# Kernel tuning notes

Hardware: AMD Instinct MI355X
Metric: run time of the kernel (lower is better)

The kernel has to match this reference:

```python
import jax, jax.numpy as jnp
import numpy as np

P = 113          # modulus; eq_token = P, vocab = P + 1
D_MODEL = 1024
D_MLP = 4096
BATCH = 16384


def setup_inputs() -> dict:
    key = jax.random.key(0)
    ks = jax.random.split(key, 9)
    return {
        "a": jax.random.randint(ks[0], (BATCH,), 0, P, dtype=jnp.int64 if jax.config.jax_enable_x64 else jnp.int32),
        "b": jax.random.randint(ks[1], (BATCH,), 0, P, dtype=jnp.int64 if jax.config.jax_enable_x64 else jnp.int32),
        "token_embed": jax.random.normal(ks[2], (P + 1, D_MODEL), dtype=jnp.float32),
        "pos_embed": jax.random.normal(ks[3], (3, D_MODEL), dtype=jnp.float32),
        "W_in_w": jax.random.normal(ks[4], (D_MLP, D_MODEL), dtype=jnp.float32) * (1.0 / np.sqrt(D_MODEL)),
        "W_in_b": jax.random.normal(ks[5], (D_MLP,), dtype=jnp.float32) * 0.02,
        "W_out_w": jax.random.normal(ks[6], (D_MODEL, D_MLP), dtype=jnp.float32) * (1.0 / np.sqrt(D_MLP)),
        "W_out_b": jax.random.normal(ks[7], (D_MODEL,), dtype=jnp.float32) * 0.02,
        "unembed_w": jax.random.normal(ks[8], (P, D_MODEL), dtype=jnp.float32) * (1.0 / np.sqrt(D_MODEL)),
    }


def reference(a, b, token_embed, pos_embed, W_in_w, W_in_b, W_out_w, W_out_b, unembed_w):
    # tokens: (batch, 3) = [a, b, eq]
    eq = jnp.full_like(a, P)
    tokens = jnp.stack([a, b, eq], axis=1)
    # embed + positional: (batch, 3, d_model)
    x = token_embed[tokens] + pos_embed[None, :, :]
    # FNet-style mixing: FFT over seq (axis 1), then over d_model (axis 2), real part
    wave = jnp.fft.fft(jnp.fft.fft(x, axis=1), axis=2).real.astype(x.dtype)
    x = x + wave
    # MLP with residual
    h = jax.nn.relu(jnp.einsum('bsd,md->bsm', x, W_in_w) + W_in_b)
    x = x + jnp.einsum('bsm,dm->bsd', h, W_out_w) + W_out_b
    # unembed only the '=' position (index 2)
    logits = jnp.einsum('bd,vd->bv', x[:, 2, :], unembed_w)
    return logits
```

## Files before the change

### kernel.cpp

```cpp
#include <hip/hip_runtime.h>

typedef __attribute__((ext_vector_type(4))) float f32x4;
typedef __attribute__((ext_vector_type(8))) short short8;

#define PMOD 113
#define NPAIR 12769
#define DM 1024
#define DMLP 4096
#define NBATCH 16384
#define SQRT3_2 0.86602540378443865f
#define CSTEP 6.1359231515425649e-3f
#define LTSTRIDE (12800 * 128)
#define NZ 8

__device__ __forceinline__ short f2bf(float x) {
    unsigned int u = __builtin_bit_cast(unsigned int, x);
    u += 0x7FFFu + ((u >> 16) & 1u);
    return (short)(u >> 16);
}
__device__ __forceinline__ float bf2f(short s) {
    return __builtin_bit_cast(float, (unsigned int)(unsigned short)s << 16);
}
__device__ __forceinline__ void cvt16(const float* p, short8& o0, short8& o1) {
    #pragma unroll
    for (int c4 = 0; c4 < 4; ++c4) {
        f32x4 v = *(const f32x4*)(p + c4 * 4);
        #pragma unroll
        for (int e = 0; e < 4; ++e) {
            short s = f2bf(v[e]);
            if (c4 < 2) o0[c4 * 4 + e] = s; else o1[(c4 - 2) * 4 + e] = s;
        }
    }
}

__global__ __launch_bounds__(256) void k_prep(
    unsigned short* __restrict__ Fb, unsigned short* __restrict__ V2b,
    unsigned short* __restrict__ Wob,
    const float* __restrict__ E, const float* __restrict__ pos,
    const float* __restrict__ Wo)
{
    __shared__ float smem[64 * 65];
    const int blk = blockIdx.x, tid = threadIdx.x;

    if (blk < 1024) {
        const int f = blk;
        for (int k = tid; k < DM; k += 256) {
            float v;
            if (k <= 512) v = cosf((float)((f * k) & 1023) * CSTEP);
            else          v = sinf((float)((f * (k - 512)) & 1023) * CSTEP);
            Fb[f * DM + k] = (unsigned short)f2bf(v);
        }
    } else if (blk < 1252) {
        const int t = blk - 1024;
        if (t >= 226) {
            for (int k = tid; k < DM; k += 256) V2b[t * DM + k] = 0;
            return;
        }
        float* vc = smem;
        float* vs = smem + 1024;
        if (t < PMOD) {
            const float* e = E + t * DM;
            const float* e2 = E + PMOD * DM;
            for (int d = tid; d < DM; d += 256) {
                float e2v = e2[d] + pos[2 * DM + d];
                vc[d] = e[d] + pos[d] - 0.5f * pos[DM + d] - 0.5f * e2v;
                vs[d] = SQRT3_2 * (pos[DM + d] - e2v);
            }
        } else {
            const float* e = E + (t - PMOD) * DM;
            for (int d = tid; d < DM; d += 256) {
                float x = e[d];
                vc[d] = -0.5f * x;
                vs[d] = SQRT3_2 * x;
            }
        }
        __syncthreads();
        for (int k = tid; k < DM; k += 256) {
            float o;
            if (k == 0)        o = vc[0];
            else if (k < 512)  o = vc[k] + vc[1024 - k];
            else if (k == 512) o = vc[512];
            else               o = vs[k - 512] - vs[1536 - k];
            V2b[t * DM + k] = (unsigned short)f2bf(o);
        }
    } else {
        const int idx = blk - 1252;
        const int m0 = (idx & 63) * 64;
        const int d0 = (idx >> 6) * 64;
        float (*tile)[65] = (float(*)[65])smem;
        #pragma unroll
        for (int it = 0; it < 16; ++it) {
            int i2 = tid + it * 256;
            int r = i2 >> 6, c = i2 & 63;
            tile[c][r] = Wo[(d0 + r) * DMLP + m0 + c];
        }
        __syncthreads();
        #pragma unroll
        for (int it = 0; it < 16; ++it) {
            int i2 = tid + it * 256;
            int r = i2 >> 6, c = i2 & 63;
            Wob[(m0 + r) * DM + d0 + c] = (unsigned short)f2bf(tile[r][c]);
        }
    }
}

template<int MODE>
__device__ __forceinline__ void mfma_body(
    int n0, int row0,
    unsigned short* __restrict__ C1, float* __restrict__ C2,
    const void* __restrict__ Av, const void* __restrict__ B1v,
    const float* __restrict__ B2, const float* __restrict__ bias,
    const float* __restrict__ E, const float* __restrict__ pos,
    const float* __restrict__ bo, short* sA, short* sB)
{
    const int tid = threadIdx.x;
    const int sr = tid >> 2, sq = (tid & 3) * 16;
    const int lane = tid & 63, w = tid >> 6;
    const int wr = w >> 1, wc = w & 1;
    const int lr = lane & 15, lg = lane >> 4;

    const unsigned short* Ab = nullptr; const float* Af = nullptr;
    {
        int r = row0 + sr;
        if (MODE == 2) { if (r < PMOD) Af = (const float*)Av + r * DM; }
        else           { if (r < 228)  Ab = (const unsigned short*)Av + r * DM; }
    }
    const unsigned short* Bb = nullptr; const float* Bf = nullptr;
    {
        int n = n0 + sr;
        if (MODE == 1) {
            if (n < 4096) Bf = (const float*)B1v + n * DM;
            else if (n - 4096 < PMOD) Bf = B2 + (n - 4096) * DM;
        } else {
            Bb = (const unsigned short*)B1v + n * DM;
        }
    }

    f32x4 acc[2][2];
    #pragma unroll
    for (int i = 0; i < 2; ++i)
        #pragma unroll
        for (int j = 0; j < 2; ++j) acc[i][j] = 0.f;

    for (int k0 = 0; k0 < DM; k0 += 64) {
        short8 a0, a1, b0, b1;
        if (MODE == 2) {
            if (Af) cvt16(Af + k0 + sq, a0, a1);
            else { a0 = 0; a1 = 0; }
        } else {
            if (Ab) { a0 = ((const short8*)(Ab + k0 + sq))[0];
                      a1 = ((const short8*)(Ab + k0 + sq))[1]; }
            else { a0 = 0; a1 = 0; }
        }
        if (MODE == 1) {
            if (Bf) cvt16(Bf + k0 + sq, b0, b1);
            else { b0 = 0; b1 = 0; }
        } else {
            b0 = ((const short8*)(Bb + k0 + sq))[0];
            b1 = ((const short8*)(Bb + k0 + sq))[1];
        }
        if (k0) __syncthreads();
        *(short8*)&sA[sr * 72 + sq] = a0;
        *(short8*)&sA[sr * 72 + sq + 8] = a1;
        *(short8*)&sB[sr * 72 + sq] = b0;
        *(short8*)&sB[sr * 72 + sq + 8] = b1;
        __syncthreads();

        #pragma unroll
        for (int ks = 0; ks < 2; ++ks) {
            short8 af[2], bfr[2];
            #pragma unroll
            for (int i = 0; i < 2; ++i)
                af[i] = *(const short8*)&sA[(wr * 32 + i * 16 + lr) * 72 + ks * 32 + lg * 8];
            #pragma unroll
            for (int j = 0; j < 2; ++j)
                bfr[j] = *(const short8*)&sB[(wc * 32 + j * 16 + lr) * 72 + ks * 32 + lg * 8];
            #pragma unroll
            for (int i = 0; i < 2; ++i)
                #pragma unroll
                for (int j = 0; j < 2; ++j)
                    acc[i][j] = __builtin_amdgcn_mfma_f32_16x16x32_bf16(af[i], bfr[j], acc[i][j], 0, 0, 0);
        }
    }

    #pragma unroll
    for (int i = 0; i < 2; ++i) {
        #pragma unroll
        for (int q = 0; q < 4; ++q) {
            int r = row0 + wr * 32 + i * 16 + lg * 4 + q;
            #pragma unroll
            for (int j = 0; j < 2; ++j) {
                int cg = n0 + wc * 32 + j * 16 + lr;
                float v = acc[i][j][q];
                if (MODE == 0) {
                    if (r < 228) {
                        if (r < PMOD) v += E[PMOD * DM + cg] + pos[2 * DM + cg];
                        if (r == 227) v += bo[cg];
                        C1[r * DM + cg] = (unsigned short)f2bf(v);
                    }
                } else if (MODE == 1) {
                    if (r < 228) {
                        if (n0 < 4096) {
                            if (r < PMOD) v += bias[cg];
                            C1[r * DMLP + cg] = (unsigned short)f2bf(v);
                        } else {
                            C2[r * 128 + cg - 4096] = v;
                        }
                    }
                } else {
                    if (r < 128) C1[r * DMLP + cg] = (unsigned short)f2bf(v);
                }
            }
        }
    }
}

__global__ __launch_bounds__(256) void k_m02(
    unsigned short* __restrict__ Tb, unsigned short* __restrict__ Mb,
    const unsigned short* __restrict__ V2b, const unsigned short* __restrict__ Fb,
    const float* __restrict__ U, const unsigned short* __restrict__ Wob,
    const float* __restrict__ E, const float* __restrict__ pos,
    const float* __restrict__ bo)
{
    __shared__ short sA[64 * 72];
    __shared__ short sB[64 * 72];
    const int blk = blockIdx.x;
    if (blk < 64) {
        mfma_body<0>((blk & 15) * 64, (blk >> 4) * 64, Tb, nullptr, V2b, Fb,
                     nullptr, nullptr, E, pos, bo, sA, sB);
    } else {
        int i = blk - 64;
        mfma_body<2>((i & 63) * 64, (i >> 6) * 64, Mb, nullptr, U, Wob,
                     nullptr, nullptr, nullptr, nullptr, nullptr, sA, sB);
    }
}

__global__ __launch_bounds__(256) void k_m1(
    unsigned short* __restrict__ Hb, float* __restrict__ L,
    const unsigned short* __restrict__ Tb, const float* __restrict__ Wi,
    const float* __restrict__ U, const float* __restrict__ bi)
{
    __shared__ short sA[64 * 72];
    __shared__ short sB[64 * 72];
    mfma_body<1>(blockIdx.x * 64, blockIdx.y * 64, Hb, L, Tb, Wi, U, bi,
                 nullptr, nullptr, nullptr, sA, sB);
}

__global__ __launch_bounds__(256) void k_pair_gemm(
    unsigned short* __restrict__ LTp,
    const unsigned short* __restrict__ Hb,
    const unsigned short* __restrict__ Mb,
    const float* __restrict__ L)
{
    __shared__ short sH[128 * 72];
    __shared__ short sM[128 * 72];

    const int tid = threadIdx.x;
    const int p0 = blockIdx.x * 128;
    const int z = blockIdx.y;
    const int kbeg = z * 512;
    const bool slice0 = (z == 0);
    unsigned short* outp = LTp + (size_t)z * LTSTRIDE;

    const int hr = tid >> 1, kh = (tid & 1) * 32;
    {
    }
    const unsigned int pc = (unsigned)min(p0 + hr, NPAIR - 1);
    const unsigned int a_r = pc / 113u;
    const unsigned int b_r = pc - a_r * 113u;
    const unsigned short* pHA = Hb + a_r * DMLP + kbeg + kh;
    const unsigned short* pHB = Hb + (PMOD + b_r) * DMLP + kbeg + kh;
    const unsigned short* pM  = Mb + hr * DMLP + kbeg + kh;

    const int lane = tid & 63, w = tid >> 6;
    const int wr = w >> 1, wc = w & 1;
    const int lr = lane & 15, lg = lane >> 4;

    f32x4 acc[4][4];
    #pragma unroll
    for (int i = 0; i < 4; ++i)
        #pragma unroll
        for (int j = 0; j < 4; ++j) acc[i][j] = 0.f;

    short8 rA[4], rB[4], rM[4];
    #pragma unroll
    for (int c = 0; c < 4; ++c) {
        rA[c] = *(const short8*)(pHA + c * 8);
        rB[c] = *(const short8*)(pHB + c * 8);
        rM[c] = *(const short8*)(pM + c * 8);
    }

    #pragma unroll 1
    for (int t = 0; t < 8; ++t) {
        short8 u[4];
        #pragma unroll
        for (int c = 0; c < 4; ++c)
            #pragma unroll
            for (int e = 0; e < 8; ++e)
                u[c][e] = f2bf(fmaxf(bf2f(rA[c][e]) + bf2f(rB[c][e]), 0.f));

        if (t) __syncthreads();
        #pragma unroll
        for (int c = 0; c < 4; ++c) {
            *(short8*)&sH[hr * 72 + kh + c * 8] = u[c];
            *(short8*)&sM[hr * 72 + kh + c * 8] = rM[c];
        }
        __syncthreads();

        if (t < 7) {
            #pragma unroll
            for (int c = 0; c < 4; ++c) {
                rA[c] = *(const short8*)(pHA + (t + 1) * 64 + c * 8);
                rB[c] = *(const short8*)(pHB + (t + 1) * 64 + c * 8);
                rM[c] = *(const short8*)(pM + (t + 1) * 64 + c * 8);
            }
        }

        #pragma unroll
        for (int ks = 0; ks < 2; ++ks) {
            short8 af[4], bf[4];
            #pragma unroll
            for (int i = 0; i < 4; ++i)
                af[i] = *(const short8*)&sH[(wr * 64 + i * 16 + lr) * 72 + ks * 32 + lg * 8];
            #pragma unroll
            for (int j = 0; j < 4; ++j)
                bf[j] = *(const short8*)&sM[(wc * 64 + j * 16 + lr) * 72 + ks * 32 + lg * 8];
            #pragma unroll
            for (int i = 0; i < 4; ++i)
                #pragma unroll
                for (int j = 0; j < 4; ++j)
                    acc[i][j] = __builtin_amdgcn_mfma_f32_16x16x32_bf16(af[i], bf[j], acc[i][j], 0, 0, 0);
        }
    }

    const float* Lb0 = L + PMOD * 128;
    const float* Lc = L + 227 * 128;
    #pragma unroll
    for (int i = 0; i < 4; ++i) {
        #pragma unroll
        for (int q = 0; q < 4; ++q) {
            int p = p0 + wr * 64 + i * 16 + lg * 4 + q;
            if (p >= NPAIR) continue;
            unsigned int pa = (unsigned)p / 113u;
            unsigned int pb = (unsigned)p - pa * 113u;
            unsigned short* dst = outp + (size_t)p * 128;
            const float* La = L + pa * 128;
            const float* Lb = Lb0 + pb * 128;
            #pragma unroll
            for (int j = 0; j < 4; ++j) {
                int col = wc * 64 + j * 16 + lr;
                float val = acc[i][j][q];
                if (slice0) val += La[col] + Lb[col] + Lc[col];
                dst[col] = (unsigned short)f2bf(val);
            }
        }
    }
}

__global__ __launch_bounds__(256) void k_gather(
    float* __restrict__ out, const unsigned short* __restrict__ LTp,
    const int* __restrict__ a, const int* __restrict__ b)
{
    int g = blockIdx.x * 256 + threadIdx.x;
    if (g >= NBATCH * PMOD) return;
    unsigned int i = (unsigned)g / 113u;
    unsigned int v = (unsigned)g - i * 113u;
    size_t off = (size_t)((unsigned)a[i] * 113u + (unsigned)b[i]) * 128 + v;
    float s = 0.f;
    #pragma unroll
    for (int z = 0; z < NZ; ++z)
        s += bf2f(LTp[(size_t)z * LTSTRIDE + off]);
    out[g] = s;
}

extern "C" void kernel_launch(void* const* d_in, const int* in_sizes, int n_in,
                              void* d_out, int out_size, void* d_ws, size_t ws_size,
                              hipStream_t stream)
{
    const int*   a   = (const int*)d_in[0];
    const int*   b   = (const int*)d_in[1];
    const float* E   = (const float*)d_in[2];
    const float* pos = (const float*)d_in[3];
    const float* Wi  = (const float*)d_in[4];
    const float* bi  = (const float*)d_in[5];
    const float* Wo  = (const float*)d_in[6];
    const float* bo  = (const float*)d_in[7];
    const float* U   = (const float*)d_in[8];
    float* out = (float*)d_out;

    unsigned short* Fb  = (unsigned short*)d_ws;
    unsigned short* V2b = Fb + 1024 * 1024;
    unsigned short* Tb  = V2b + 228 * 1024;
    unsigned short* Hb  = Tb + 228 * 1024;
    unsigned short* Wob = Hb + 228 * 4096;
    unsigned short* Mb  = Wob + 4096 * 1024;
    unsigned short* LTp = Mb + 128 * 4096;
    float* L = (float*)(LTp + NZ * LTSTRIDE);

    k_prep<<<2276, 256, 0, stream>>>(Fb, V2b, Wob, E, pos, Wo);
    k_m02<<<192, 256, 0, stream>>>(Tb, Mb, V2b, Fb, U, Wob, E, pos, bo);
    k_m1<<<dim3(66, 4), 256, 0, stream>>>(Hb, L, Tb, Wi, U, bi);
    k_pair_gemm<<<dim3(100, NZ), 256, 0, stream>>>(LTp, Hb, Mb, L);
    k_gather<<<(NBATCH * PMOD + 255) / 256, 256, 0, stream>>>(out, LTp, a, b);

    (void)in_sizes; (void)n_in; (void)out_size; (void)ws_size;
}
```

Baseline: 176.7 us.

## Pre-convert Wi/U to bf16, split-K the first MLP GEMM, and interleave partial-logit layout

Moves fp32-to-bf16 conversion of W_in and unembed into the prep kernel so the GEMM inner loops load bf16 directly. Splits the k_m1 GEMM into four K-slices for more blocks (264 to 1056) and adds a reduction kernel that sums the partials, adds the bias and writes Hb and L. Reorders the pair-GEMM output so the NZ partial slices of each pair are contiguous, and rewrites the gather to read them with 16-byte vector loads. This trades an extra kernel launch and fp32 partial-buffer traffic for better occupancy and more coalesced gathers.

```diff
diff --git a/kernel.cpp b/kernel.cpp
--- a/kernel.cpp
+++ b/kernel.cpp
@@ -2,6 +2,7 @@
 
 typedef __attribute__((ext_vector_type(4))) float f32x4;
 typedef __attribute__((ext_vector_type(8))) short short8;
+typedef __attribute__((ext_vector_type(4))) unsigned short us4;
 
 #define PMOD 113
 #define NPAIR 12769
@@ -10,8 +11,8 @@
 #define NBATCH 16384
 #define SQRT3_2 0.86602540378443865f
 #define CSTEP 6.1359231515425649e-3f
-#define LTSTRIDE (12800 * 128)
 #define NZ 8
+#define HPELEMS (228 * 4224)
 
 __device__ __forceinline__ short f2bf(float x) {
     unsigned int u = __builtin_bit_cast(unsigned int, x);
@@ -35,9 +36,11 @@
 
 __global__ __launch_bounds__(256) void k_prep(
     unsigned short* __restrict__ Fb, unsigned short* __restrict__ V2b,
-    unsigned short* __restrict__ Wob,
+    unsigned short* __restrict__ Wob, unsigned short* __restrict__ Wib,
+    unsigned short* __restrict__ Ub,
     const float* __restrict__ E, const float* __restrict__ pos,
-    const float* __restrict__ Wo)
+    const float* __restrict__ Wo, const float* __restrict__ Wi,
+    const float* __restrict__ U)
 {
     __shared__ float smem[64 * 65];
     const int blk = blockIdx.x, tid = threadIdx.x;
@@ -83,7 +86,7 @@
             else               o = vs[k - 512] - vs[1536 - k];
             V2b[t * DM + k] = (unsigned short)f2bf(o);
         }
-    } else {
+    } else if (blk < 2276) {
         const int idx = blk - 1252;
         const int m0 = (idx & 63) * 64;
         const int d0 = (idx >> 6) * 64;
@@ -101,15 +104,29 @@
             int r = i2 >> 6, c = i2 & 63;
             Wob[(m0 + r) * DM + d0 + c] = (unsigned short)f2bf(tile[r][c]);
         }
+    } else if (blk < 3300) {
+        const int eb = (blk - 2276) * 4096 + tid * 16;
+        short8 o0, o1;
+        cvt16(Wi + eb, o0, o1);
+        *(short8*)&Wib[eb] = o0;
+        *(short8*)&Wib[eb + 8] = o1;
+    } else {
+        const int eb = (blk - 3300) * 4096 + tid * 16;
+        if (eb < PMOD * DM) {
+            short8 o0, o1;
+            cvt16(U + eb, o0, o1);
+            *(short8*)&Ub[eb] = o0;
+            *(short8*)&Ub[eb + 8] = o1;
+        }
     }
 }
 
 template<int MODE>
 __device__ __forceinline__ void mfma_body(
-    int n0, int row0,
-    unsigned short* __restrict__ C1, float* __restrict__ C2,
-    const void* __restrict__ Av, const void* __restrict__ B1v,
-    const float* __restrict__ B2, const float* __restrict__ bias,
+    int n0, int row0, int kbeg, int kend, int Arows,
+    unsigned short* __restrict__ C1, float* __restrict__ C2f,
+    const unsigned short* __restrict__ A, const unsigned short* __restrict__ B1,
+    const unsigned short* __restrict__ B2,
     const float* __restrict__ E, const float* __restrict__ pos,
     const float* __restrict__ bo, short* sA, short* sB)
 {
@@ -119,20 +136,16 @@
     const int wr = w >> 1, wc = w & 1;
     const int lr = lane & 15, lg = lane >> 4;
 
-    const unsigned short* Ab = nullptr; const float* Af = nullptr;
-    {
-        int r = row0 + sr;
-        if (MODE == 2) { if (r < PMOD) Af = (const float*)Av + r * DM; }
-        else           { if (r < 228)  Ab = (const unsigned short*)Av + r * DM; }
-    }
-    const unsigned short* Bb = nullptr; const float* Bf = nullptr;
+    const unsigned short* Ab = (row0 + sr < Arows) ? (A + (row0 + sr) * DM) : nullptr;
+    const unsigned short* Bb;
     {
         int n = n0 + sr;
         if (MODE == 1) {
-            if (n < 4096) Bf = (const float*)B1v + n * DM;
-            else if (n - 4096 < PMOD) Bf = B2 + (n - 4096) * DM;
+            if (n < 4096) Bb = B1 + n * DM;
+            else if (n - 4096 < PMOD) Bb = B2 + (n - 4096) * DM;
+            else Bb = nullptr;
         } else {
-            Bb = (const unsigned short*)B1v + n * DM;
+            Bb = B1 + n * DM;
         }
     }
 
@@ -142,24 +155,15 @@
         #pragma unroll
         for (int j = 0; j < 2; ++j) acc[i][j] = 0.f;
 
-    for (int k0 = 0; k0 < DM; k0 += 64) {
+    for (int k0 = kbeg; k0 < kend; k0 += 64) {
         short8 a0, a1, b0, b1;
-        if (MODE == 2) {
-            if (Af) cvt16(Af + k0 + sq, a0, a1);
-            else { a0 = 0; a1 = 0; }
-        } else {
-            if (Ab) { a0 = ((const short8*)(Ab + k0 + sq))[0];
-                      a1 = ((const short8*)(Ab + k0 + sq))[1]; }
-            else { a0 = 0; a1 = 0; }
-        }
-        if (MODE == 1) {
-            if (Bf) cvt16(Bf + k0 + sq, b0, b1);
-            else { b0 = 0; b1 = 0; }
-        } else {
-            b0 = ((const short8*)(Bb + k0 + sq))[0];
-            b1 = ((const short8*)(Bb + k0 + sq))[1];
-        }
-        if (k0) __syncthreads();
+        if (Ab) { a0 = ((const short8*)(Ab + k0 + sq))[0];
+                  a1 = ((const short8*)(Ab + k0 + sq))[1]; }
+        else { a0 = 0; a1 = 0; }
+        if (Bb) { b0 = ((const short8*)(Bb + k0 + sq))[0];
+                  b1 = ((const short8*)(Bb + k0 + sq))[1]; }
+        else { b0 = 0; b1 = 0; }
+        if (k0 != kbeg) __syncthreads();
         *(short8*)&sA[sr * 72 + sq] = a0;
         *(short8*)&sA[sr * 72 + sq + 8] = a1;
         *(short8*)&sB[sr * 72 + sq] = b0;
@@ -199,14 +203,7 @@
                         C1[r * DM + cg] = (unsigned short)f2bf(v);
                     }
                 } else if (MODE == 1) {
-                    if (r < 228) {
-                        if (n0 < 4096) {
-                            if (r < PMOD) v += bias[cg];
-                            C1[r * DMLP + cg] = (unsigned short)f2bf(v);
-                        } else {
-                            C2[r * 128 + cg - 4096] = v;
-                        }
-                    }
+                    if (r < 228) C2f[r * 4224 + cg] = v;
                 } else {
                     if (r < 128) C1[r * DMLP + cg] = (unsigned short)f2bf(v);
                 }
@@ -218,7 +215,7 @@
 __global__ __launch_bounds__(256) void k_m02(
     unsigned short* __restrict__ Tb, unsigned short* __restrict__ Mb,
     const unsigned short* __restrict__ V2b, const unsigned short* __restrict__ Fb,
-    const float* __restrict__ U, const unsigned short* __restrict__ Wob,
+    const unsigned short* __restrict__ Ub, const unsigned short* __restrict__ Wob,
     const float* __restrict__ E, const float* __restrict__ pos,
     const float* __restrict__ bo)
 {
@@ -226,24 +223,48 @@
     __shared__ short sB[64 * 72];
     const int blk = blockIdx.x;
     if (blk < 64) {
-        mfma_body<0>((blk & 15) * 64, (blk >> 4) * 64, Tb, nullptr, V2b, Fb,
-                     nullptr, nullptr, E, pos, bo, sA, sB);
+        mfma_body<0>((blk & 15) * 64, (blk >> 4) * 64, 0, DM, 228, Tb, nullptr,
+                     V2b, Fb, nullptr, E, pos, bo, sA, sB);
     } else {
         int i = blk - 64;
-        mfma_body<2>((i & 63) * 64, (i >> 6) * 64, Mb, nullptr, U, Wob,
-                     nullptr, nullptr, nullptr, nullptr, nullptr, sA, sB);
+        mfma_body<2>((i & 63) * 64, (i >> 6) * 64, 0, DM, PMOD, Mb, nullptr,
+                     Ub, Wob, nullptr, nullptr, nullptr, nullptr, sA, sB);
     }
 }
 
 __global__ __launch_bounds__(256) void k_m1(
-    unsigned short* __restrict__ Hb, float* __restrict__ L,
-    const unsigned short* __restrict__ Tb, const float* __restrict__ Wi,
-    const float* __restrict__ U, const float* __restrict__ bi)
+    float* __restrict__ Hp,
+    const unsigned short* __restrict__ Tb, const unsigned short* __restrict__ Wib,
+    const unsigned short* __restrict__ Ub)
 {
     __shared__ short sA[64 * 72];
     __shared__ short sB[64 * 72];
-    mfma_body<1>(blockIdx.x * 64, blockIdx.y * 64, Hb, L, Tb, Wi, U, bi,
-                 nullptr, nullptr, nullptr, sA, sB);
+    const int kbeg = blockIdx.z * 256;
+    mfma_body<1>(blockIdx.x * 64, blockIdx.y * 64, kbeg, kbeg + 256, 228,
+                 nullptr, Hp + (size_t)blockIdx.z * HPELEMS,
+                 Tb, Wib, Ub, nullptr, nullptr, nullptr, sA, sB);
+}
+
+__global__ __launch_bounds__(256) void k_hred(
+    unsigned short* __restrict__ Hb, float* __restrict__ L,
+    const float* __restrict__ Hp, const float* __restrict__ bi)
+{
+    const int e = (blockIdx.x * 256 + threadIdx.x) * 4;
+    if (e >= HPELEMS) return;
+    f32x4 s = *(const f32x4*)(Hp + e);
+    #pragma unroll
+    for (int z = 1; z < 4; ++z) s += *(const f32x4*)(Hp + (size_t)z * HPELEMS + e);
+    unsigned int row = (unsigned)e / 4224u;
+    unsigned int col = (unsigned)e - row * 4224u;
+    if (col < 4096) {
+        if (row < PMOD) s += *(const f32x4*)(bi + col);
+        us4 o;
+        #pragma unroll
+        for (int j = 0; j < 4; ++j) o[j] = (unsigned short)f2bf(s[j]);
+        *(us4*)&Hb[row * DMLP + col] = o;
+    } else {
+        *(f32x4*)&L[row * 128 + (col - 4096)] = s;
+    }
 }
 
 __global__ __launch_bounds__(256) void k_pair_gemm(
@@ -260,11 +281,8 @@
     const int z = blockIdx.y;
     const int kbeg = z * 512;
     const bool slice0 = (z == 0);
-    unsigned short* outp = LTp + (size_t)z * LTSTRIDE;
 
     const int hr = tid >> 1, kh = (tid & 1) * 32;
-    {
-    }
     const unsigned int pc = (unsigned)min(p0 + hr, NPAIR - 1);
     const unsigned int a_r = pc / 113u;
     const unsigned int b_r = pc - a_r * 113u;
@@ -343,7 +361,7 @@
             if (p >= NPAIR) continue;
             unsigned int pa = (unsigned)p / 113u;
             unsigned int pb = (unsigned)p - pa * 113u;
-            unsigned short* dst = outp + (size_t)p * 128;
+            unsigned short* dst = LTp + ((size_t)p * NZ + z) * 128;
             const float* La = L + pa * 128;
             const float* Lb = Lb0 + pb * 128;
             #pragma unroll
@@ -361,16 +379,25 @@
     float* __restrict__ out, const unsigned short* __restrict__ LTp,
     const int* __restrict__ a, const int* __restrict__ b)
 {
-    int g = blockIdx.x * 256 + threadIdx.x;
-    if (g >= NBATCH * PMOD) return;
-    unsigned int i = (unsigned)g / 113u;
-    unsigned int v = (unsigned)g - i * 113u;
-    size_t off = (size_t)((unsigned)a[i] * 113u + (unsigned)b[i]) * 128 + v;
-    float s = 0.f;
-    #pragma unroll
-    for (int z = 0; z < NZ; ++z)
-        s += bf2f(LTp[(size_t)z * LTSTRIDE + off]);
-    out[g] = s;
+    const int tid = threadIdx.x;
+    const int elem = blockIdx.x * 16 + (tid >> 4);
+    const int t16 = tid & 15;
+    const int v0 = t16 * 8;
+    if (v0 > 112) return;
+    unsigned int pair = (unsigned)a[elem] * 113u + (unsigned)b[elem];
+    const unsigned short* src = LTp + (size_t)pair * (NZ * 128) + v0;
+    float s[8];
+    #pragma unroll
+    for (int e = 0; e < 8; ++e) s[e] = 0.f;
+    #pragma unroll
+    for (int z = 0; z < NZ; ++z) {
+        short8 vv = *(const short8*)(src + z * 128);
+        #pragma unroll
+        for (int e = 0; e < 8; ++e) s[e] += bf2f(vv[e]);
+    }
+    float* o = out + (size_t)elem * PMOD + v0;
+    const int nv = (v0 + 8 <= PMOD) ? 8 : (PMOD - v0);
+    for (int e = 0; e < nv; ++e) o[e] = s[e];
 }
 
 extern "C" void kernel_launch(void* const* d_in, const int* in_sizes, int n_in,
@@ -394,14 +421,18 @@
     unsigned short* Hb  = Tb + 228 * 1024;
     unsigned short* Wob = Hb + 228 * 4096;
     unsigned short* Mb  = Wob + 4096 * 1024;
-    unsigned short* LTp = Mb + 128 * 4096;
-    float* L = (float*)(LTp + NZ * LTSTRIDE);
-
-    k_prep<<<2276, 256, 0, stream>>>(Fb, V2b, Wob, E, pos, Wo);
-    k_m02<<<192, 256, 0, stream>>>(Tb, Mb, V2b, Fb, U, Wob, E, pos, bo);
-    k_m1<<<dim3(66, 4), 256, 0, stream>>>(Hb, L, Tb, Wi, U, bi);
+    unsigned short* Wib = Mb + 128 * 4096;
+    unsigned short* Ub  = Wib + 4096 * 1024;
+    unsigned short* LTp = Ub + 116 * 1024;
+    float* L  = (float*)(LTp + (size_t)12800 * NZ * 128);
+    float* Hp = L + 228 * 128;
+
+    k_prep<<<3329, 256, 0, stream>>>(Fb, V2b, Wob, Wib, Ub, E, pos, Wo, Wi, U);
+    k_m02<<<192, 256, 0, stream>>>(Tb, Mb, V2b, Fb, Ub, Wob, E, pos, bo);
+    k_m1<<<dim3(66, 4, 4), 256, 0, stream>>>(Hp, Tb, Wib, Ub);
+    k_hred<<<(HPELEMS / 4 + 255) / 256, 256, 0, stream>>>(Hb, L, Hp, bi);
     k_pair_gemm<<<dim3(100, NZ), 256, 0, stream>>>(LTp, Hb, Mb, L);
-    k_gather<<<(NBATCH * PMOD + 255) / 256, 256, 0, stream>>>(out, LTp, a, b);
+    k_gather<<<NBATCH / 16, 256, 0, stream>>>(out, LTp, a, b);
 
     (void)in_sizes; (void)n_in; (void)out_size; (void)ws_size;
 }
```

After: 171.6 us. 2.9% less time.
